# Performance work log

Measured on AMD Instinct MI355X. Metric: run time of the kernel, lower is better.

Reference implementation:

```python
import jax, jax.numpy as jnp
import numpy as np

T_STEPS = 10       # T_pos = T_neg = 10 hardcoded in forward
ATTN_SCALE = 0.125 # scale hardcoded in forward (not head_dim**-0.5)
V_TH = 1.0         # spikingjelly IFNode defaults: v_threshold=1.0, v_reset=0.0 (hard reset)
SG_ALPHA = 4.0     # default Sigmoid surrogate alpha

@jax.custom_vjp
def spike(v):
    return (v >= 0.0).astype(v.dtype)

def _spike_fwd(v):
    return spike(v), v

def _spike_bwd(v, g):
    sg = jax.nn.sigmoid(SG_ALPHA * v)
    return (g * SG_ALPHA * sg * (1.0 - sg),)

spike.defvjp(_spike_fwd, _spike_bwd)

def if_node_const_input(y, T=T_STEPS):
    """Multi-step IF neuron driven by the SAME input y at every step.
    charge: v += y; fire: s = H(v - 1); hard reset: v = (1 - s) * v.
    Returns spikes of shape [T, *y.shape]."""
    def step(v, _):
        v = v + y
        s = spike(v - V_TH)
        v = (1.0 - s) * v
        return v, s
    _, spikes = jax.lax.scan(step, jnp.zeros_like(y), None, length=T)
    return spikes

def setup_inputs() -> dict:
    key = jax.random.key(0)
    ks = jax.random.split(key, 6)
    N, C = 2048, 2048
    x = jax.random.normal(ks[0], (N, C), dtype=jnp.float32)
    freqs_cis = jax.random.normal(ks[1], (N, 64), dtype=jnp.float32)  # unused by forward
    w_scale = 0.02
    wq = jax.random.normal(ks[2], (C, C), dtype=jnp.float32) * w_scale
    wk = jax.random.normal(ks[3], (C, C), dtype=jnp.float32) * w_scale
    wv = jax.random.normal(ks[4], (C, C), dtype=jnp.float32) * w_scale
    wo = jax.random.normal(ks[5], (C, C), dtype=jnp.float32) * w_scale
    return {"x": x, "freqs_cis": freqs_cis, "wq": wq, "wk": wk, "wv": wv, "wo": wo}

def reference(x, freqs_cis, wq, wk, wv, wo):
    N, C = x.shape
    n_heads, head_dim = 16, 128  # C == n_heads * head_dim; n_kv_heads == n_heads so repeat_kv is a no-op
    T = T_STEPS

    x_pos = jax.nn.relu(x)
    x_neg = jax.nn.relu(-x)

    # Input is identical at every timestep, so apply the linear once, then run IF over T.
    def branch(xb):
        q = if_node_const_input(xb @ wq)  # [T, N, C] binary spikes
        k = if_node_const_input(xb @ wk)
        v = if_node_const_input(xb @ wv)
        return q, k, v

    qp, kp, vp = branch(x_pos)
    qn, kn, vn = branch(x_neg)
    xq = (qp - qn).reshape(T, N, n_heads, head_dim)
    xk = (kp - kn).reshape(T, N, n_heads, head_dim)
    xv = (vp - vn).reshape(T, N, n_heads, head_dim)

    # no-softmax attention over the HEAD axis, per token: [T,N,H,H]
    attn = jnp.einsum('tnhd,tnmd->tnhm', xq, xk) * ATTN_SCALE
    x_attn = jnp.einsum('tnhm,tnmd->tnhd', attn, xv)          # [T,N,H,Dh]
    x_attn = jnp.swapaxes(x_attn, -1, -2).reshape(T, N, C)    # transpose(-1,-2) then merge

    xo = x_attn @ wo  # [T, N, C]
    return xo.mean(axis=0)
```

## Files before the change

kernel.cpp:

```cpp
#include <hip/hip_runtime.h>
#include <hip/hip_bf16.h>


#define LIST_CAP (512u * 1024u)
#define FLAG_EPS 4e-4f

typedef __attribute__((ext_vector_type(8))) short short8;
typedef __attribute__((ext_vector_type(16))) float floatx16;

__device__ const unsigned d_LUT[16] = {0u, 0x3FFu, 0x2AAu, 0x124u, 0x88u,
                                       0x210u, 0x20u, 0x40u, 0x80u, 0x100u,
                                       0x200u, 0u, 0u, 0u, 0u, 0u};

__device__ __forceinline__ void bf16x2_rne(float a, unsigned& p1, unsigned& p2) {
  const unsigned u = __float_as_uint(a);
  const unsigned t1 = u + 0x7FFFu + ((u >> 16) & 1u);
  p1 = t1 >> 16;
  const float r = a - __uint_as_float(t1 & 0xFFFF0000u);
  const unsigned u2 = __float_as_uint(r);
  p2 = (u2 + 0x7FFFu + ((u2 >> 16) & 1u)) >> 16;
}

__device__ __forceinline__ int frag_off(int c, int r) {
  return (((c >> 1) * 4 + (r >> 5)) * 2 + (c & 1)) * 256 + (r & 31) * 8;
}

template <int ZERO_CNT>
__global__ __launch_bounds__(256) void wsplit(
    const float* __restrict__ W0, const float* __restrict__ W1,
    const float* __restrict__ W2, unsigned short* __restrict__ Bpk,
    int NCT, unsigned* __restrict__ cnt) {
  if (ZERO_CNT && blockIdx.x == 0 && blockIdx.y == 0 && threadIdx.x == 0)
    *cnt = 0u;
  __shared__ float Wf[32 * 132];
  const int ct = blockIdx.x, k0 = blockIdx.y * 32;
  const int c0 = ct * 128;
  const int sel = c0 >> 11;
  const float* W = (sel == 0) ? W0 : ((sel == 1) ? W1 : W2);
  const int cc0 = c0 & 2047;
  const int t = threadIdx.x;

  const int kr = t >> 3, cq = (t & 7) * 16;
#pragma unroll
  for (int u = 0; u < 4; u++) {
    const float4 v = *(const float4*)(W + (size_t)(k0 + kr) * 2048 + cc0 + cq + 4 * u);
    *(float4*)&Wf[kr * 132 + cq + 4 * u] = v;
  }
  __syncthreads();

  const int cc = t >> 1, ch0 = (t & 1) * 2;
  unsigned short* img1 = Bpk + ((size_t)(0 * NCT + ct) * 64 + blockIdx.y) * 4096;
  unsigned short* img2 = Bpk + ((size_t)(1 * NCT + ct) * 64 + blockIdx.y) * 4096;
#pragma unroll
  for (int c = ch0; c < ch0 + 2; c++) {
    unsigned q1[8], q2[8];
#pragma unroll
    for (int e = 0; e < 8; e++) bf16x2_rne(Wf[(c * 8 + e) * 132 + cc], q1[e], q2[e]);
    const int off = frag_off(c, cc);
    uint4 P1, P2;
    P1.x = q1[0] | (q1[1] << 16); P1.y = q1[2] | (q1[3] << 16);
    P1.z = q1[4] | (q1[5] << 16); P1.w = q1[6] | (q1[7] << 16);
    P2.x = q2[0] | (q2[1] << 16); P2.y = q2[2] | (q2[3] << 16);
    P2.z = q2[4] | (q2[5] << 16); P2.w = q2[6] | (q2[7] << 16);
    *(uint4*)&img1[off] = P1;
    *(uint4*)&img2[off] = P2;
  }
}

template <int RELU>
__global__ __launch_bounds__(256) void asplit(
    const float* __restrict__ src, unsigned short* __restrict__ Apk, int NRT) {
  const int rt = blockIdx.x, k0i = blockIdx.y;
  const int t = threadIdx.x;
  const int r = t >> 1, half = t & 1;
  int grow = rt * 128 + r;
  float sgn = 1.f;
  if (RELU && grow >= 2048) { grow -= 2048; sgn = -1.f; }
  const float* s = src + (size_t)grow * 2048 + k0i * 32 + half * 16;
  float f[16];
#pragma unroll
  for (int u = 0; u < 4; u++) {
    const float4 v = *(const float4*)(s + 4 * u);
    f[4 * u + 0] = v.x; f[4 * u + 1] = v.y;
    f[4 * u + 2] = v.z; f[4 * u + 3] = v.w;
  }
  if (RELU) {
#pragma unroll
    for (int e = 0; e < 16; e++) f[e] = fmaxf(sgn * f[e], 0.f);
  }
  unsigned q1[16], q2[16];
#pragma unroll
  for (int e = 0; e < 16; e++) bf16x2_rne(f[e], q1[e], q2[e]);

  unsigned short* img1 = Apk + ((size_t)(0 * NRT + rt) * 64 + k0i) * 4096;
  unsigned short* img2 = Apk + ((size_t)(1 * NRT + rt) * 64 + k0i) * 4096;
#pragma unroll
  for (int cc = 0; cc < 2; cc++) {
    const int c = half * 2 + cc;
    const int off = frag_off(c, r);
    const int e0 = cc * 8;
    uint4 P1, P2;
    P1.x = q1[e0 + 0] | (q1[e0 + 1] << 16); P1.y = q1[e0 + 2] | (q1[e0 + 3] << 16);
    P1.z = q1[e0 + 4] | (q1[e0 + 5] << 16); P1.w = q1[e0 + 6] | (q1[e0 + 7] << 16);
    P2.x = q2[e0 + 0] | (q2[e0 + 1] << 16); P2.y = q2[e0 + 2] | (q2[e0 + 3] << 16);
    P2.z = q2[e0 + 4] | (q2[e0 + 5] << 16); P2.w = q2[e0 + 6] | (q2[e0 + 7] << 16);
    *(uint4*)&img1[off] = P1;
    *(uint4*)&img2[off] = P2;
  }
}

template <int MODE>
__global__ __launch_bounds__(256, 4) void gemm_dma(
    const unsigned short* __restrict__ Apk, const unsigned short* __restrict__ Bpk,
    int NRT, int NCT, unsigned char* __restrict__ MaskJ,
    unsigned* __restrict__ list, unsigned* __restrict__ cnt,
    float* __restrict__ Out) {
  __shared__ unsigned short sh[4][4096];

  const int tid = threadIdx.x;
  const int bx = blockIdx.x, by = blockIdx.y;
  const int lane = tid & 63, wave = tid >> 6;
  const int wr = wave >> 1, wc = wave & 1;
  const int lm = lane & 31, lg = lane >> 5;

  const unsigned short* gsrc =
      (wave < 2) ? (Apk + ((size_t)(wave * NRT + by) * 64) * 4096)
                 : (Bpk + ((size_t)((wave - 2) * NCT + bx) * 64) * 4096);

  floatx16 acc[2][2];
#pragma unroll
  for (int i = 0; i < 2; i++)
#pragma unroll
    for (int j = 0; j < 2; j++)
#pragma unroll
      for (int e = 0; e < 16; e++) acc[i][j][e] = 0.f;

  for (int k0i = 0; k0i < 64; k0i++) {
    __syncthreads();
    const unsigned short* gp = gsrc + (size_t)k0i * 4096;
#pragma unroll
    for (int i = 0; i < 8; i++) {
      __builtin_amdgcn_global_load_lds(
          (const __attribute__((address_space(1))) unsigned*)(gp + i * 512 + lane * 8),
          (__attribute__((address_space(3))) unsigned*)(&sh[wave][i * 512]), 16, 0, 0);
    }
    __syncthreads();

#pragma unroll
    for (int ks = 0; ks < 2; ks++) {
      short8 a1[2], a2[2], b1[2], b2[2];
#pragma unroll
      for (int it = 0; it < 2; it++) {
        const int off = ((ks * 4 + 2 * wr + it) * 2 + lg) * 256 + lm * 8;
        a1[it] = *(const short8*)&sh[0][off];
        a2[it] = *(const short8*)&sh[1][off];
      }
#pragma unroll
      for (int jt = 0; jt < 2; jt++) {
        const int off = ((ks * 4 + 2 * wc + jt) * 2 + lg) * 256 + lm * 8;
        b1[jt] = *(const short8*)&sh[2][off];
        b2[jt] = *(const short8*)&sh[3][off];
      }
#pragma unroll
      for (int it = 0; it < 2; it++)
#pragma unroll
        for (int jt = 0; jt < 2; jt++)
          acc[it][jt] = __builtin_amdgcn_mfma_f32_32x32x16_bf16(
              a1[it], b1[jt], acc[it][jt], 0, 0, 0);
#pragma unroll
      for (int it = 0; it < 2; it++)
#pragma unroll
        for (int jt = 0; jt < 2; jt++)
          acc[it][jt] = __builtin_amdgcn_mfma_f32_32x32x16_bf16(
              a1[it], b2[jt], acc[it][jt], 0, 0, 0);
#pragma unroll
      for (int it = 0; it < 2; it++)
#pragma unroll
        for (int jt = 0; jt < 2; jt++)
          acc[it][jt] = __builtin_amdgcn_mfma_f32_32x32x16_bf16(
              a2[it], b1[jt], acc[it][jt], 0, 0, 0);
    }
  }

#pragma unroll
  for (int it = 0; it < 2; it++) {
#pragma unroll
    for (int jt = 0; jt < 2; jt++) {
      const int gn = bx * 128 + 64 * wc + 32 * jt + lm;
#pragma unroll
      for (int reg = 0; reg < 16; reg++) {
        const int gm = by * 128 + 64 * wr + 32 * it + (reg & 3) + 8 * (reg >> 2) + 4 * lg;
        const float y = acc[it][jt][reg];
        if (MODE == 1) {
          Out[(size_t)gm * 2048 + gn] = y * 0.1f;
        } else {
          float r = __builtin_amdgcn_rcpf(y);
          r = fminf(fmaxf(r, -1.0f), 12.0f);
          const float jf = floorf(r);
          const float d0 = fmaf(jf, y, -1.0f);
          const float i0 = fminf(fmaxf(jf, 1.0f), 10.0f);
          const float i1 = fminf(fmaxf(jf + 1.0f, 1.0f), 10.0f);
          const float e0 = fmaf(i0, y, -1.0f);
          const float e1 = fmaf(i1, y, -1.0f);
          const float mind = fminf(fabsf(e0), fabsf(e1));
          const unsigned J = (unsigned)(int)((d0 >= 0.0f) ? jf : jf + 1.0f);
          MaskJ[(size_t)gm * 6144 + gn] = (unsigned char)((J <= 10u) ? J : 0u);
          if (mind < FLAG_EPS) {
            const unsigned idx = atomicAdd(cnt, 1u);
            if (idx < LIST_CAP) list[idx] = ((unsigned)gm << 13) | (unsigned)gn;
          }
        }
      }
    }
  }
}

__global__ __launch_bounds__(256) void transpose_w(
    const float* __restrict__ W0, const float* __restrict__ W1,
    const float* __restrict__ W2, float* __restrict__ WT) {
  __shared__ float tile[32][33];
  const int k0 = blockIdx.x * 32;
  const int c0 = blockIdx.y * 32;
  const int sel = c0 >> 11;
  const float* W = (sel == 0) ? W0 : ((sel == 1) ? W1 : W2);
  const int cc0 = c0 & 2047;
  const int tx = threadIdx.x, ty = threadIdx.y;
#pragma unroll
  for (int rep = 0; rep < 4; rep++)
    tile[ty + 8 * rep][tx] = W[(size_t)(k0 + ty + 8 * rep) * 2048 + cc0 + tx];
  __syncthreads();
#pragma unroll
  for (int rep = 0; rep < 4; rep++)
    WT[(size_t)(c0 + ty + 8 * rep) * 2048 + k0 + tx] = tile[tx][ty + 8 * rep];
}

__global__ __launch_bounds__(256) void rescue(
    const float* __restrict__ X, const float* __restrict__ WT,
    const unsigned* __restrict__ list, const unsigned* __restrict__ cnt,
    unsigned char* __restrict__ MaskJ) {
  const unsigned nItems = min(*cnt, LIST_CAP);
  const unsigned gtid = blockIdx.x * blockDim.x + threadIdx.x;
  const unsigned wave = gtid >> 6, lane = gtid & 63;
  const unsigned nWaves = (gridDim.x * blockDim.x) >> 6;

  for (unsigned i = wave; i < nItems; i += nWaves) {
    const unsigned e = list[i];
    const int r = (int)(e >> 13), c = (int)(e & 8191u);
    const float* xrow = X + (size_t)((r < 2048) ? r : r - 2048) * 2048;
    const float sg = (r < 2048) ? 1.f : -1.f;
    const float* wrow = WT + (size_t)c * 2048;
    double s = 0.0;
#pragma unroll
    for (int it = 0; it < 8; it++) {
      const int k = (it * 64 + (int)lane) * 4;
      const float4 xv = *(const float4*)(xrow + k);
      const float4 wv = *(const float4*)(wrow + k);
      const float a0 = fmaxf(sg * xv.x, 0.f);
      const float a1 = fmaxf(sg * xv.y, 0.f);
      const float a2 = fmaxf(sg * xv.z, 0.f);
      const float a3 = fmaxf(sg * xv.w, 0.f);
      s += (double)a0 * (double)wv.x + (double)a1 * (double)wv.y +
           (double)a2 * (double)wv.z + (double)a3 * (double)wv.w;
    }
#pragma unroll
    for (int off = 32; off > 0; off >>= 1) s += __shfl_down(s, off);
    if (lane == 0) {
      double v = 0.0;
      unsigned J = 0;
#pragma unroll
      for (int t = 0; t < 10; t++) {
        v += s;
        if (J == 0u && v >= 1.0) J = (unsigned)(t + 1);
      }
      MaskJ[(size_t)r * 6144 + c] = (unsigned char)J;
    }
  }
}

__global__ __launch_bounds__(256) void spike_attn(const unsigned char* __restrict__ MaskJ,
                                                  float* __restrict__ xbar) {
  const int n = blockIdx.x;
  const int tid = threadIdx.x;
  const int lane = tid & 63;

  __shared__ unsigned long long qpB[16][2], qnB[16][2], kpB[16][2], knB[16][2];
  __shared__ float xvT[16 * 132];
  __shared__ float attnS[16 * 17];
  __shared__ unsigned lutS[16];

  if (tid < 16) lutS[tid] = d_LUT[tid];
  __syncthreads();

  const unsigned char* mp = MaskJ + (size_t)n * 6144;
  const unsigned char* mn = MaskJ + (size_t)(n + 2048) * 6144;

  unsigned q_p[8], q_n[8], k_p[8], k_n[8], v_p[8], v_n[8];
#pragma unroll
  for (int j = 0; j < 8; j++) {
    const int c = tid + 256 * j;
    q_p[j] = lutS[mp[c]];        q_n[j] = lutS[mn[c]];
    k_p[j] = lutS[mp[2048 + c]]; k_n[j] = lutS[mn[2048 + c]];
    v_p[j] = lutS[mp[4096 + c]]; v_n[j] = lutS[mn[4096 + c]];
  }

  float acc[8];
#pragma unroll
  for (int j = 0; j < 8; j++) acc[j] = 0.f;

  for (int t = 0; t < 10; t++) {
#pragma unroll
    for (int j = 0; j < 8; j++) {
      const int c = tid + 256 * j;
      const unsigned long long bqp = __ballot((q_p[j] >> t) & 1u);
      const unsigned long long bqn = __ballot((q_n[j] >> t) & 1u);
      const unsigned long long bkp = __ballot((k_p[j] >> t) & 1u);
      const unsigned long long bkn = __ballot((k_n[j] >> t) & 1u);
      const int h = c >> 7, word = (c >> 6) & 1;
      if (lane == 0) {
        qpB[h][word] = bqp; qnB[h][word] = bqn;
        kpB[h][word] = bkp; knB[h][word] = bkn;
      }
      const int m = h, d = c & 127;
      xvT[m * 132 + d] =
          (float)((v_p[j] >> t) & 1u) - (float)((v_n[j] >> t) & 1u);
    }
    __syncthreads();

    {
      const int h = tid >> 4, m = tid & 15;
      int dot = 0;
#pragma unroll
      for (int w = 0; w < 2; w++) {
        const unsigned long long qp = qpB[h][w], qn = qnB[h][w];
        const unsigned long long kp = kpB[m][w], kn = knB[m][w];
        dot += __popcll(qp & kp) + __popcll(qn & kn) -
               __popcll(qp & kn) - __popcll(qn & kp);
      }
      attnS[h * 17 + m] = (float)dot * 0.125f;
    }
    __syncthreads();

    {
      const int h = tid & 15;
      float arow[16];
#pragma unroll
      for (int m = 0; m < 16; m++) arow[m] = attnS[h * 17 + m];
#pragma unroll
      for (int j = 0; j < 8; j++) {
        const int d = (tid + 256 * j) >> 4;
        float s = 0.f;
#pragma unroll
        for (int m = 0; m < 16; m++) s += arow[m] * xvT[m * 132 + d];
        acc[j] += s;
      }
    }
    __syncthreads();
  }

#pragma unroll
  for (int j = 0; j < 8; j++) xbar[(size_t)n * 2048 + tid + 256 * j] = acc[j];
}

extern "C" void kernel_launch(void* const* d_in, const int* in_sizes, int n_in,
                              void* d_out, int out_size, void* d_ws, size_t ws_size,
                              hipStream_t stream) {
  const float* x = (const float*)d_in[0];
  const float* wq = (const float*)d_in[2];
  const float* wk = (const float*)d_in[3];
  const float* wv = (const float*)d_in[4];
  const float* wo = (const float*)d_in[5];
  float* out = (float*)d_out;

  char* ws = (char*)d_ws;
  unsigned char* MaskJ = (unsigned char*)ws;
  unsigned short* WOpk = (unsigned short*)ws;
  char* reg2 = ws + (size_t)4096 * 6144;
  unsigned short* Bpk = (unsigned short*)reg2;
  float* WT = (float*)reg2;
  unsigned short* Xbpk = (unsigned short*)reg2;
  char* reg3 = reg2 + (size_t)6144 * 2048 * 2 * 2;
  unsigned short* Apk = (unsigned short*)reg3;
  float* xbar = (float*)reg3;
  unsigned* list = (unsigned*)(reg3 + (size_t)4096 * 2048 * 2 * 2);
  unsigned* cnt = list + LIST_CAP;

  wsplit<1><<<dim3(48, 64), 256, 0, stream>>>(wq, wk, wv, Bpk, 48, cnt);
  asplit<1><<<dim3(32, 64), 256, 0, stream>>>(x, Apk, 32);
  gemm_dma<0><<<dim3(48, 32), 256, 0, stream>>>(Apk, Bpk, 32, 48, MaskJ, list, cnt, nullptr);
  transpose_w<<<dim3(64, 192), dim3(32, 8), 0, stream>>>(wq, wk, wv, WT);
  rescue<<<2048, 256, 0, stream>>>(x, WT, list, cnt, MaskJ);
  spike_attn<<<2048, 256, 0, stream>>>(MaskJ, xbar);
  wsplit<0><<<dim3(16, 64), 256, 0, stream>>>(wo, wo, wo, WOpk, 16, nullptr);
  asplit<0><<<dim3(16, 64), 256, 0, stream>>>(xbar, Xbpk, 16);
  gemm_dma<1><<<dim3(16, 16), 256, 0, stream>>>(Xbpk, WOpk, 16, 16, nullptr, nullptr, nullptr, out);
}
```

Measured before the change: 796.3 us.

## Load GEMM fragments directly from global into registers with double buffering

Replaces the LDS-staged GEMM (global_load_lds plus two barriers per k-step) with per-wave direct global loads of pre-packed MFMA fragments into registers. A two-deep register ping-pong prefetches the next k-slice while MFMAs run on the current one, and the barriers go away. The cost is that each wave now loads its own A and B fragments, so tiles shared across waves are fetched redundantly from L2 instead of once into LDS. Register pressure also rises, which is why launch bounds drop from 4 to 3 blocks per CU.

```diff
diff --git a/kernel.cpp b/kernel.cpp
--- a/kernel.cpp
+++ b/kernel.cpp
@@ -23,6 +23,10 @@
 
 __device__ __forceinline__ int frag_off(int c, int r) {
   return (((c >> 1) * 4 + (r >> 5)) * 2 + (c & 1)) * 256 + (r & 31) * 8;
+}
+
+__device__ __forceinline__ short8 gld(const unsigned short* p) {
+  return *(const short8*)p;
 }
 
 template <int ZERO_CNT>
@@ -109,23 +113,48 @@
   }
 }
 
+__device__ __forceinline__ void mfma_set12(floatx16 (&acc)[2][2],
+    const short8 (&A1)[2], const short8 (&A2)[2],
+    const short8 (&B1)[2], const short8 (&B2)[2]) {
+#pragma unroll
+  for (int it = 0; it < 2; it++)
+#pragma unroll
+    for (int jt = 0; jt < 2; jt++)
+      acc[it][jt] = __builtin_amdgcn_mfma_f32_32x32x16_bf16(A1[it], B1[jt], acc[it][jt], 0, 0, 0);
+#pragma unroll
+  for (int it = 0; it < 2; it++)
+#pragma unroll
+    for (int jt = 0; jt < 2; jt++)
+      acc[it][jt] = __builtin_amdgcn_mfma_f32_32x32x16_bf16(A1[it], B2[jt], acc[it][jt], 0, 0, 0);
+#pragma unroll
+  for (int it = 0; it < 2; it++)
+#pragma unroll
+    for (int jt = 0; jt < 2; jt++)
+      acc[it][jt] = __builtin_amdgcn_mfma_f32_32x32x16_bf16(A2[it], B1[jt], acc[it][jt], 0, 0, 0);
+}
+
+#define LOADSET(S, off)                                              \
+  S##A1[0] = gld(bA1 + (off)); S##A1[1] = gld(bA1 + (off) + 512);    \
+  S##A2[0] = gld(bA2 + (off)); S##A2[1] = gld(bA2 + (off) + 512);    \
+  S##B1[0] = gld(bB1 + (off)); S##B1[1] = gld(bB1 + (off) + 512);    \
+  S##B2[0] = gld(bB2 + (off)); S##B2[1] = gld(bB2 + (off) + 512);
+
 template <int MODE>
-__global__ __launch_bounds__(256, 4) void gemm_dma(
+__global__ __launch_bounds__(256, 3) void gemm_reg(
     const unsigned short* __restrict__ Apk, const unsigned short* __restrict__ Bpk,
     int NRT, int NCT, unsigned char* __restrict__ MaskJ,
     unsigned* __restrict__ list, unsigned* __restrict__ cnt,
     float* __restrict__ Out) {
-  __shared__ unsigned short sh[4][4096];
-
   const int tid = threadIdx.x;
   const int bx = blockIdx.x, by = blockIdx.y;
   const int lane = tid & 63, wave = tid >> 6;
   const int wr = wave >> 1, wc = wave & 1;
   const int lm = lane & 31, lg = lane >> 5;
 
-  const unsigned short* gsrc =
-      (wave < 2) ? (Apk + ((size_t)(wave * NRT + by) * 64) * 4096)
-                 : (Bpk + ((size_t)((wave - 2) * NCT + bx) * 64) * 4096);
+  const unsigned short* bA1 = Apk + ((size_t)(0 * NRT + by) * 64) * 4096 + 2 * wr * 512 + lane * 8;
+  const unsigned short* bA2 = Apk + ((size_t)(1 * NRT + by) * 64) * 4096 + 2 * wr * 512 + lane * 8;
+  const unsigned short* bB1 = Bpk + ((size_t)(0 * NCT + bx) * 64) * 4096 + 2 * wc * 512 + lane * 8;
+  const unsigned short* bB2 = Bpk + ((size_t)(1 * NCT + bx) * 64) * 4096 + 2 * wc * 512 + lane * 8;
 
   floatx16 acc[2][2];
 #pragma unroll
@@ -135,51 +164,19 @@
 #pragma unroll
       for (int e = 0; e < 16; e++) acc[i][j][e] = 0.f;
 
-  for (int k0i = 0; k0i < 64; k0i++) {
-    __syncthreads();
-    const unsigned short* gp = gsrc + (size_t)k0i * 4096;
-#pragma unroll
-    for (int i = 0; i < 8; i++) {
-      __builtin_amdgcn_global_load_lds(
-          (const __attribute__((address_space(1))) unsigned*)(gp + i * 512 + lane * 8),
-          (__attribute__((address_space(3))) unsigned*)(&sh[wave][i * 512]), 16, 0, 0);
-    }
-    __syncthreads();
-
-#pragma unroll
-    for (int ks = 0; ks < 2; ks++) {
-      short8 a1[2], a2[2], b1[2], b2[2];
-#pragma unroll
-      for (int it = 0; it < 2; it++) {
-        const int off = ((ks * 4 + 2 * wr + it) * 2 + lg) * 256 + lm * 8;
-        a1[it] = *(const short8*)&sh[0][off];
-        a2[it] = *(const short8*)&sh[1][off];
-      }
-#pragma unroll
-      for (int jt = 0; jt < 2; jt++) {
-        const int off = ((ks * 4 + 2 * wc + jt) * 2 + lg) * 256 + lm * 8;
-        b1[jt] = *(const short8*)&sh[2][off];
-        b2[jt] = *(const short8*)&sh[3][off];
-      }
-#pragma unroll
-      for (int it = 0; it < 2; it++)
-#pragma unroll
-        for (int jt = 0; jt < 2; jt++)
-          acc[it][jt] = __builtin_amdgcn_mfma_f32_32x32x16_bf16(
-              a1[it], b1[jt], acc[it][jt], 0, 0, 0);
-#pragma unroll
-      for (int it = 0; it < 2; it++)
-#pragma unroll
-        for (int jt = 0; jt < 2; jt++)
-          acc[it][jt] = __builtin_amdgcn_mfma_f32_32x32x16_bf16(
-              a1[it], b2[jt], acc[it][jt], 0, 0, 0);
-#pragma unroll
-      for (int it = 0; it < 2; it++)
-#pragma unroll
-        for (int jt = 0; jt < 2; jt++)
-          acc[it][jt] = __builtin_amdgcn_mfma_f32_32x32x16_bf16(
-              a2[it], b1[jt], acc[it][jt], 0, 0, 0);
-    }
+  short8 PA1[2], PA2[2], PB1[2], PB2[2];
+  short8 QA1[2], QA2[2], QB1[2], QB2[2];
+
+  LOADSET(P, 0)
+  for (int s = 0; s < 128; s += 2) {
+    const size_t o1 = (size_t)(s + 1) * 2048;
+    LOADSET(Q, o1)
+    mfma_set12(acc, PA1, PA2, PB1, PB2);
+    if (s + 2 < 128) {
+      const size_t o2 = (size_t)(s + 2) * 2048;
+      LOADSET(P, o2)
+    }
+    mfma_set12(acc, QA1, QA2, QB1, QB2);
   }
 
 #pragma unroll
@@ -386,11 +383,11 @@
 
   wsplit<1><<<dim3(48, 64), 256, 0, stream>>>(wq, wk, wv, Bpk, 48, cnt);
   asplit<1><<<dim3(32, 64), 256, 0, stream>>>(x, Apk, 32);
-  gemm_dma<0><<<dim3(48, 32), 256, 0, stream>>>(Apk, Bpk, 32, 48, MaskJ, list, cnt, nullptr);
+  gemm_reg<0><<<dim3(48, 32), 256, 0, stream>>>(Apk, Bpk, 32, 48, MaskJ, list, cnt, nullptr);
   transpose_w<<<dim3(64, 192), dim3(32, 8), 0, stream>>>(wq, wk, wv, WT);
   rescue<<<2048, 256, 0, stream>>>(x, WT, list, cnt, MaskJ);
   spike_attn<<<2048, 256, 0, stream>>>(MaskJ, xbar);
   wsplit<0><<<dim3(16, 64), 256, 0, stream>>>(wo, wo, wo, WOpk, 16, nullptr);
   asplit<0><<<dim3(16, 64), 256, 0, stream>>>(xbar, Xbpk, 16);
-  gemm_dma<1><<<dim3(16, 16), 256, 0, stream>>>(Xbpk, WOpk, 16, 16, nullptr, nullptr, nullptr, out);
-}
+  gemm_reg<1><<<dim3(16, 16), 256, 0, stream>>>(Xbpk, WOpk, 16, 16, nullptr, nullptr, nullptr, out);
+}
```

Result: slower. 859.4 us (+7.9%).

## Replace synchronous GEMM K-loop with triple-buffered async LDS ring pipeline

Applied to the files above, without the earlier changes.

The bf16-split GEMM previously loaded each 64-wide K chunk into LDS and then synchronized twice per iteration, so global loads and MFMA work never overlapped. It is now a 3-slot ring of half-size chunks with two chunks prefetched ahead via global_load_lds and gated by vmcnt waits, plus one barrier per step. It also uses explicit ds_read_b128 with precomputed offsets and raises wave priority around the MFMA block. LDS use grows to 48KB per block and occupancy is lowered to 3 blocks per CU, and the tail re-issues loads for the last chunk, which costs some redundant traffic.

```diff
diff --git a/kernel.cpp b/kernel.cpp
--- a/kernel.cpp
+++ b/kernel.cpp
@@ -23,6 +23,16 @@
 
 __device__ __forceinline__ int frag_off(int c, int r) {
   return (((c >> 1) * 4 + (r >> 5)) * 2 + (c & 1)) * 256 + (r & 31) * 8;
+}
+
+__device__ __forceinline__ unsigned lds_addr32(const void* p) {
+  return (unsigned)(size_t)(const __attribute__((address_space(3))) char*)p;
+}
+
+__device__ __forceinline__ short8 ds_read_b128a(unsigned addr) {
+  short8 r;
+  asm volatile("ds_read_b128 %0, %1" : "=v"(r) : "v"(addr));
+  return r;
 }
 
 template <int ZERO_CNT>
@@ -110,12 +120,12 @@
 }
 
 template <int MODE>
-__global__ __launch_bounds__(256, 4) void gemm_dma(
+__global__ __launch_bounds__(256, 3) void gemm_ring(
     const unsigned short* __restrict__ Apk, const unsigned short* __restrict__ Bpk,
-    int NRT, int NCT, unsigned char* __restrict__ MaskJ,
+    int NRT, int NCT, int NCH, unsigned char* __restrict__ MaskJ,
     unsigned* __restrict__ list, unsigned* __restrict__ cnt,
     float* __restrict__ Out) {
-  __shared__ unsigned short sh[4][4096];
+  __shared__ unsigned short sh[3 * 8192];
 
   const int tid = threadIdx.x;
   const int bx = blockIdx.x, by = blockIdx.y;
@@ -123,9 +133,20 @@
   const int wr = wave >> 1, wc = wave & 1;
   const int lm = lane & 31, lg = lane >> 5;
 
-  const unsigned short* gsrc =
-      (wave < 2) ? (Apk + ((size_t)(wave * NRT + by) * 64) * 4096)
-                 : (Bpk + ((size_t)((wave - 2) * NCT + bx) * 64) * 4096);
+  const unsigned short* gbase =
+      (wave < 2) ? (Apk + ((size_t)(wave * NRT + by) * (NCH >> 1)) * 4096)
+                 : (Bpk + ((size_t)((wave - 2) * NCT + bx) * (NCH >> 1)) * 4096);
+
+  auto issue4 = [&](int c, int slot) {
+    const unsigned short* g = gbase + (size_t)c * 2048 + lane * 8;
+#pragma unroll
+    for (int i = 0; i < 4; i++)
+      __builtin_amdgcn_global_load_lds(
+          (const __attribute__((address_space(1))) unsigned*)(g + i * 512),
+          (__attribute__((address_space(3))) unsigned*)(
+              &sh[slot * 8192 + wave * 2048 + i * 512]),
+          16, 0, 0);
+  };
 
   floatx16 acc[2][2];
 #pragma unroll
@@ -135,52 +156,62 @@
 #pragma unroll
       for (int e = 0; e < 16; e++) acc[i][j][e] = 0.f;
 
-  for (int k0i = 0; k0i < 64; k0i++) {
-    __syncthreads();
-    const unsigned short* gp = gsrc + (size_t)k0i * 4096;
-#pragma unroll
-    for (int i = 0; i < 8; i++) {
-      __builtin_amdgcn_global_load_lds(
-          (const __attribute__((address_space(1))) unsigned*)(gp + i * 512 + lane * 8),
-          (__attribute__((address_space(3))) unsigned*)(&sh[wave][i * 512]), 16, 0, 0);
-    }
-    __syncthreads();
-
-#pragma unroll
-    for (int ks = 0; ks < 2; ks++) {
-      short8 a1[2], a2[2], b1[2], b2[2];
-#pragma unroll
-      for (int it = 0; it < 2; it++) {
-        const int off = ((ks * 4 + 2 * wr + it) * 2 + lg) * 256 + lm * 8;
-        a1[it] = *(const short8*)&sh[0][off];
-        a2[it] = *(const short8*)&sh[1][off];
-      }
-#pragma unroll
-      for (int jt = 0; jt < 2; jt++) {
-        const int off = ((ks * 4 + 2 * wc + jt) * 2 + lg) * 256 + lm * 8;
-        b1[jt] = *(const short8*)&sh[2][off];
-        b2[jt] = *(const short8*)&sh[3][off];
-      }
-#pragma unroll
-      for (int it = 0; it < 2; it++)
-#pragma unroll
-        for (int jt = 0; jt < 2; jt++)
-          acc[it][jt] = __builtin_amdgcn_mfma_f32_32x32x16_bf16(
-              a1[it], b1[jt], acc[it][jt], 0, 0, 0);
-#pragma unroll
-      for (int it = 0; it < 2; it++)
-#pragma unroll
-        for (int jt = 0; jt < 2; jt++)
-          acc[it][jt] = __builtin_amdgcn_mfma_f32_32x32x16_bf16(
-              a1[it], b2[jt], acc[it][jt], 0, 0, 0);
-#pragma unroll
-      for (int it = 0; it < 2; it++)
-#pragma unroll
-        for (int jt = 0; jt < 2; jt++)
-          acc[it][jt] = __builtin_amdgcn_mfma_f32_32x32x16_bf16(
-              a2[it], b1[jt], acc[it][jt], 0, 0, 0);
-    }
-  }
+  const unsigned aoff0 = (unsigned)((((2 * wr + 0) * 2 + lg) * 256 + lm * 8) * 2);
+  const unsigned aoff1 = (unsigned)((((2 * wr + 1) * 2 + lg) * 256 + lm * 8) * 2);
+  const unsigned boff0 = (unsigned)((((2 * wc + 0) * 2 + lg) * 256 + lm * 8) * 2);
+  const unsigned boff1 = (unsigned)((((2 * wc + 1) * 2 + lg) * 256 + lm * 8) * 2);
+  const unsigned shbase = lds_addr32(&sh[0]);
+
+  issue4(0, 0);
+  issue4(1, 1);
+
+  int slot = 0;
+  for (int c = 0; c < NCH; c++) {
+    asm volatile("s_waitcnt vmcnt(4)" ::: "memory");
+    __builtin_amdgcn_s_barrier();
+    __builtin_amdgcn_sched_barrier(0);
+    {
+      const int cn = c + 2;
+      int snxt = slot + 2; if (snxt >= 3) snxt -= 3;
+      issue4((cn < NCH) ? cn : (NCH - 1), snxt);
+    }
+    const unsigned sb = shbase + (unsigned)(slot * 16384);
+    short8 a1[2], a2[2], b1[2], b2[2];
+    a1[0] = ds_read_b128a(sb + aoff0);
+    a1[1] = ds_read_b128a(sb + aoff1);
+    a2[0] = ds_read_b128a(sb + 4096u + aoff0);
+    a2[1] = ds_read_b128a(sb + 4096u + aoff1);
+    b1[0] = ds_read_b128a(sb + 8192u + boff0);
+    b1[1] = ds_read_b128a(sb + 8192u + boff1);
+    b2[0] = ds_read_b128a(sb + 12288u + boff0);
+    b2[1] = ds_read_b128a(sb + 12288u + boff1);
+    asm volatile("s_waitcnt lgkmcnt(0)" ::: "memory");
+    __builtin_amdgcn_sched_barrier(0);
+    __builtin_amdgcn_s_setprio(1);
+#pragma unroll
+    for (int it = 0; it < 2; it++)
+#pragma unroll
+      for (int jt = 0; jt < 2; jt++)
+        acc[it][jt] = __builtin_amdgcn_mfma_f32_32x32x16_bf16(
+            a1[it], b1[jt], acc[it][jt], 0, 0, 0);
+#pragma unroll
+    for (int it = 0; it < 2; it++)
+#pragma unroll
+      for (int jt = 0; jt < 2; jt++)
+        acc[it][jt] = __builtin_amdgcn_mfma_f32_32x32x16_bf16(
+            a1[it], b2[jt], acc[it][jt], 0, 0, 0);
+#pragma unroll
+    for (int it = 0; it < 2; it++)
+#pragma unroll
+      for (int jt = 0; jt < 2; jt++)
+        acc[it][jt] = __builtin_amdgcn_mfma_f32_32x32x16_bf16(
+            a2[it], b1[jt], acc[it][jt], 0, 0, 0);
+    __builtin_amdgcn_s_setprio(0);
+    slot = (slot == 2) ? 0 : slot + 1;
+  }
+
+  asm volatile("s_waitcnt vmcnt(0)" ::: "memory");
+  __builtin_amdgcn_sched_barrier(0);
 
 #pragma unroll
   for (int it = 0; it < 2; it++) {
@@ -386,11 +417,11 @@
 
   wsplit<1><<<dim3(48, 64), 256, 0, stream>>>(wq, wk, wv, Bpk, 48, cnt);
   asplit<1><<<dim3(32, 64), 256, 0, stream>>>(x, Apk, 32);
-  gemm_dma<0><<<dim3(48, 32), 256, 0, stream>>>(Apk, Bpk, 32, 48, MaskJ, list, cnt, nullptr);
+  gemm_ring<0><<<dim3(48, 32), 256, 0, stream>>>(Apk, Bpk, 32, 48, 128, MaskJ, list, cnt, nullptr);
   transpose_w<<<dim3(64, 192), dim3(32, 8), 0, stream>>>(wq, wk, wv, WT);
   rescue<<<2048, 256, 0, stream>>>(x, WT, list, cnt, MaskJ);
   spike_attn<<<2048, 256, 0, stream>>>(MaskJ, xbar);
   wsplit<0><<<dim3(16, 64), 256, 0, stream>>>(wo, wo, wo, WOpk, 16, nullptr);
   asplit<0><<<dim3(16, 64), 256, 0, stream>>>(xbar, Xbpk, 16);
-  gemm_dma<1><<<dim3(16, 16), 256, 0, stream>>>(Xbpk, WOpk, 16, 16, nullptr, nullptr, nullptr, out);
-}
+  gemm_ring<1><<<dim3(16, 16), 256, 0, stream>>>(Xbpk, WOpk, 16, 16, 128, nullptr, nullptr, nullptr, out);
+}
```

Result: faster. 770.3 us (-3.3%).
